# Kernel tuning notes

Hardware: AMD Instinct MI355X
Metric: run time of the kernel (lower is better)

Reference implementation:

```python
import jax, jax.numpy as jnp
import numpy as np

# ---- config (matches init_kwargs) ----
SPATIAL_SCALE = 0.0625
POOLED = 7
OUT_DIM = 256
SAMPLE_PER_PART = 4
TRANS_STD = 0.1
PART_SIZE = 7
DEFORM_FC_DIM = 1024
# group_size == 1 -> position-sensitive group index is always 0, channel c == ctop


def _deform_roi_pool(feat, rois, offset, no_trans):
    """Faithful JAX port of DeformablePSROIPoolForward (DCNv2), group_size=1.
    feat: (B,C,H,W), rois: (N,5)=[b,x1,y1,x2,y2], offset: (N,2,P,P) or None.
    Returns (N,C,P,P)."""
    B, C, H, W = feat.shape
    N = rois.shape[0]
    P, S = POOLED, SAMPLE_PER_PART
    dt = feat.dtype
    featT = jnp.transpose(feat, (0, 2, 3, 1))  # (B,H,W,C) for spatial gathers

    b = rois[:, 0].astype(jnp.int32)
    rsw = jnp.round(rois[:, 1]) * SPATIAL_SCALE - 0.5
    rsh = jnp.round(rois[:, 2]) * SPATIAL_SCALE - 0.5
    rew = (jnp.round(rois[:, 3]) + 1.0) * SPATIAL_SCALE - 0.5
    reh = (jnp.round(rois[:, 4]) + 1.0) * SPATIAL_SCALE - 0.5
    roi_w = jnp.maximum(rew - rsw, 0.1)
    roi_h = jnp.maximum(reh - rsh, 0.1)
    bin_h = roi_h / P            # (N,)
    bin_w = roi_w / P
    sub_h = bin_h / S
    sub_w = bin_w / S

    ph = jnp.arange(P)
    pw = jnp.arange(P)
    part_h = jnp.floor(ph.astype(dt) / P * PART_SIZE).astype(jnp.int32)  # == ph when part_size==P
    part_w = jnp.floor(pw.astype(dt) / P * PART_SIZE).astype(jnp.int32)

    if no_trans:
        tx = jnp.zeros((N, P, P), dt)
        ty = jnp.zeros((N, P, P), dt)
    else:
        tx = offset[:, 0][:, part_h][:, :, part_w] * TRANS_STD  # (N,P,P)
        ty = offset[:, 1][:, part_h][:, :, part_w] * TRANS_STD

    hstart = ph.astype(dt)[None, :, None] * bin_h[:, None, None] + rsh[:, None, None] + ty * roi_h[:, None, None]
    wstart = pw.astype(dt)[None, None, :] * bin_w[:, None, None] + rsw[:, None, None] + tx * roi_w[:, None, None]

    ih = jnp.arange(S).astype(dt)
    iw = jnp.arange(S).astype(dt)
    # sample coords, shape (N,P,P,S,S); ih along axis -2, iw along axis -1
    h = hstart[..., None, None] + ih[:, None] * sub_h[:, None, None, None, None]
    w = wstart[..., None, None] + iw[None, :] * sub_w[:, None, None, None, None]

    valid = (w >= -0.5) & (w <= W - 0.5) & (h >= -0.5) & (h <= H - 0.5)
    hc = jnp.clip(h, 0.0, H - 1.0)
    wc = jnp.clip(w, 0.0, W - 1.0)
    h0 = jnp.floor(hc).astype(jnp.int32)
    w0 = jnp.floor(wc).astype(jnp.int32)
    h1 = jnp.minimum(h0 + 1, H - 1)
    w1 = jnp.minimum(w0 + 1, W - 1)
    lh = hc - h0.astype(dt)
    lw = wc - w0.astype(dt)

    bidx = b[:, None, None, None, None]

    def g(yy, xx):  # (N,P,P,S,S,C)
        return featT[bidx, yy, xx]

    val = (g(h0, w0) * ((1 - lh) * (1 - lw))[..., None]
           + g(h0, w1) * ((1 - lh) * lw)[..., None]
           + g(h1, w0) * (lh * (1 - lw))[..., None]
           + g(h1, w1) * (lh * lw)[..., None])
    val = jnp.where(valid[..., None], val, jnp.zeros((), dt))
    ssum = val.sum(axis=(3, 4))                       # (N,P,P,C)
    cnt = valid.sum(axis=(3, 4)).astype(dt)           # (N,P,P)
    out = jnp.where(cnt[..., None] > 0, ssum / jnp.maximum(cnt, 1.0)[..., None], jnp.zeros((), dt))
    return jnp.transpose(out, (0, 3, 1, 2))           # (N,C,P,P)


def setup_inputs() -> dict:
    key = jax.random.key(0)
    ks = jax.random.split(key, 12)
    B, C, H, W = 2, OUT_DIM, 100, 100
    N = 512
    img = H / SPATIAL_SCALE  # 1600

    feat = jax.random.normal(ks[0], (B, C, H, W), jnp.float32)

    bi = jax.random.randint(ks[1], (N,), 0, B).astype(jnp.float32)
    x1 = jax.random.uniform(ks[2], (N,), jnp.float32, 0.0, img - 420.0)
    y1 = jax.random.uniform(ks[3], (N,), jnp.float32, 0.0, img - 420.0)
    x2 = x1 + jax.random.uniform(ks[4], (N,), jnp.float32, 32.0, 400.0)
    y2 = y1 + jax.random.uniform(ks[5], (N,), jnp.float32, 32.0, 400.0)
    rois = jnp.stack([bi, x1, y1, x2, y2], axis=1)

    fin = POOLED * POOLED * OUT_DIM  # 12544
    w1 = jax.random.normal(ks[6], (DEFORM_FC_DIM, fin), jnp.float32) / np.sqrt(fin)
    b1 = jnp.zeros((DEFORM_FC_DIM,), jnp.float32)
    w2 = jax.random.normal(ks[7], (DEFORM_FC_DIM, DEFORM_FC_DIM), jnp.float32) / np.sqrt(DEFORM_FC_DIM)
    b2 = jnp.zeros((DEFORM_FC_DIM,), jnp.float32)
    # original init zeroes the last layer; use small random so offsets/mask are non-trivial
    w3 = jax.random.normal(ks[8], (POOLED * POOLED * 3, DEFORM_FC_DIM), jnp.float32) * 0.01
    b3 = jnp.zeros((POOLED * POOLED * 3,), jnp.float32)
    return {"input": feat, "rois": rois, "w1": w1, "b1": b1, "w2": w2, "b2": b2, "w3": w3, "b3": b3}


def reference(input, rois, w1, b1, w2, b2, w3, b3):
    N = rois.shape[0]
    P = POOLED
    # pass 1: plain (no_trans) deformable RoI pooling to predict offsets/mask
    roi0 = _deform_roi_pool(input, rois, None, no_trans=True)      # (N,C,P,P)
    x = roi0.reshape(N, -1)
    x = jax.nn.relu(x @ w1.T + b1)
    x = jax.nn.relu(x @ w2.T + b2)
    om = (x @ w3.T + b3).reshape(N, 3, P, P)
    offset = om[:, 0:2]                                            # (N,2,P,P) [trans_x, trans_y]
    mask = jax.nn.sigmoid(om[:, 2:3])                              # (N,1,P,P)
    # pass 2: deformable pooling with learned offsets, modulated by mask
    out = _deform_roi_pool(input, rois, offset, no_trans=False) * mask
    return out
```

## Files before the change

kernel.cpp:

```cpp
#include <hip/hip_runtime.h>

#define BB 2
#define CC 256
#define HH 100
#define WW 100
#define NROI 512
#define KDIM 12544
#define FC 1024

typedef _Float16 half_t;
typedef _Float16 f16x2 __attribute__((ext_vector_type(2)));
typedef _Float16 f16x8 __attribute__((ext_vector_type(8)));
typedef _Float16 f16x4 __attribute__((ext_vector_type(4)));
typedef float f32x4 __attribute__((ext_vector_type(4)));

__device__ __forceinline__ void gload16(const half_t* g, half_t* l) {
  __builtin_amdgcn_global_load_lds(
      (const __attribute__((address_space(1))) unsigned int*)g,
      (__attribute__((address_space(3))) unsigned int*)l, 16, 0, 0);
}

__global__ __launch_bounds__(256) void prep0(const float* __restrict__ feat,
                                             half_t* __restrict__ featT,
                                             const float* __restrict__ w2,
                                             half_t* __restrict__ w2h) {
  int bid = blockIdx.x;
  if (bid >= 5008) {
    int i4 = ((bid - 5008) * 256 + threadIdx.x) * 4;
    float4 v = *(const float4*)(w2 + i4);
    f16x4 o;
    o[0] = (half_t)v.x; o[1] = (half_t)v.y; o[2] = (half_t)v.z; o[3] = (half_t)v.w;
    *(f16x4*)(w2h + i4) = o;
    return;
  }
  __shared__ float tile[32][33];
  const int bx = bid % 313;
  const int rem = bid / 313;
  const int by = rem & 7;
  const int bz = rem >> 3;
  const int tx = threadIdx.x & 31, ty = threadIdx.x >> 5;
  const int hw0 = bx * 32;
  const int c0 = by * 32;
  const float* fb = feat + (size_t)bz * CC * (HH * WW);
#pragma unroll
  for (int i = 0; i < 4; i++) {
    int c = c0 + ty + i * 8;
    int hw = hw0 + tx;
    tile[ty + i * 8][tx] = (hw < HH * WW) ? fb[(size_t)c * (HH * WW) + hw] : 0.0f;
  }
  __syncthreads();
  half_t* ob = featT + (size_t)bz * (HH * WW) * CC;
#pragma unroll
  for (int i = 0; i < 4; i++) {
    int hw = hw0 + ty + i * 8;
    int c = c0 + tx;
    if (hw < HH * WW) ob[(size_t)hw * CC + c] = (half_t)tile[tx][ty + i * 8];
  }
}

struct PixW { int idx; float w; };

template <bool PASS2>
__global__ __launch_bounds__(512) void pool_kernel(const half_t* __restrict__ featT,
                                                   const float* __restrict__ rois,
                                                   const float* __restrict__ part3,
                                                   const float* __restrict__ b3,
                                                   half_t* __restrict__ xout,
                                                   float* __restrict__ out,
                                                   const float* __restrict__ w1,
                                                   half_t* __restrict__ w1h) {
  __shared__ __align__(16) PixW s_pix[49 * 32];
  __shared__ int s_cnt[49];
  __shared__ float s_scale[49];
  __shared__ float  s_outf[PASS2 ? KDIM : 1];
  __shared__ half_t s_outh[PASS2 ? 1 : KDIM];

  const int n = blockIdx.x;
  const int tid = threadIdx.x;
  if (!PASS2 && n >= NROI) {
    int i4 = ((n - NROI) * 512 + tid) * 4;
    float4 v = *(const float4*)(w1 + i4);
    f16x4 o;
    o[0] = (half_t)v.x; o[1] = (half_t)v.y; o[2] = (half_t)v.z; o[3] = (half_t)v.w;
    *(f16x4*)(w1h + i4) = o;
    return;
  }
  const float* r = rois + n * 5;
  const int b = (int)r[0];
  const float rsw = rintf(r[1]) * 0.0625f - 0.5f;
  const float rsh = rintf(r[2]) * 0.0625f - 0.5f;
  const float rew = (rintf(r[3]) + 1.0f) * 0.0625f - 0.5f;
  const float reh = (rintf(r[4]) + 1.0f) * 0.0625f - 0.5f;
  const float roi_w = fmaxf(rew - rsw, 0.1f);
  const float roi_h = fmaxf(reh - rsh, 0.1f);
  const float bin_h = roi_h / 7.0f, bin_w = roi_w / 7.0f;
  const float sub_h = bin_h * 0.25f, sub_w = bin_w * 0.25f;
  const half_t* fb = featT + (size_t)b * (HH * WW) * CC;

  if (tid < 49) {
    const int p = tid, ph = p / 7, pw = p - ph * 7;
    float tx = 0.0f, ty = 0.0f, mask = 1.0f;
    if (PASS2) {
      float o0 = b3[p], o1 = b3[49 + p], o2 = b3[98 + p];
#pragma unroll
      for (int zz = 0; zz < 8; zz++) {
        const float* pz = part3 + ((size_t)zz * NROI + n) * 147;
        o0 += pz[p]; o1 += pz[49 + p]; o2 += pz[98 + p];
      }
      tx = o0 * 0.1f;
      ty = o1 * 0.1f;
      mask = 1.0f / (1.0f + expf(-o2));
    }
    const float hst = (float)ph * bin_h + rsh + ty * roi_h;
    const float wst = (float)pw * bin_w + rsw + tx * roi_w;
    float wh[6] = {0, 0, 0, 0, 0, 0};
    float hc0 = fminf(fmaxf(hst, 0.0f), 99.0f);
    const int r0 = (int)hc0;
    int rtop = r0;
    float vsh = 0.0f;
#pragma unroll
    for (int i = 0; i < 4; i++) {
      float h = hst + (float)i * sub_h;
      bool v = (h >= -0.5f) && (h <= (float)HH - 0.5f);
      float hc = fminf(fmaxf(h, 0.0f), 99.0f);
      int h0 = (int)hc;
      float lh = hc - (float)h0;
      int h1 = min(h0 + 1, HH - 1);
      if (v) { wh[h0 - r0] += 1.0f - lh; wh[h1 - r0] += lh; vsh += 1.0f; }
      rtop = h1;
    }
    float wwc[6] = {0, 0, 0, 0, 0, 0};
    float wc0 = fminf(fmaxf(wst, 0.0f), 99.0f);
    const int c0 = (int)wc0;
    int ctop = c0;
    float vsw = 0.0f;
#pragma unroll
    for (int j = 0; j < 4; j++) {
      float w = wst + (float)j * sub_w;
      bool v = (w >= -0.5f) && (w <= (float)WW - 0.5f);
      float wc = fminf(fmaxf(w, 0.0f), 99.0f);
      int w0 = (int)wc;
      float lw = wc - (float)w0;
      int w1_ = min(w0 + 1, WW - 1);
      if (v) { wwc[w0 - c0] += 1.0f - lw; wwc[w1_ - c0] += lw; vsw += 1.0f; }
      ctop = w1_;
    }
    const int nr = rtop - r0 + 1, nc = ctop - c0 + 1;
    float cntf = vsh * vsw;
    s_scale[p] = (cntf > 0.0f) ? mask / cntf : 0.0f;
    PixW* dst = &s_pix[p * 32];
    int m = 0;
    for (int ri = 0; ri < nr; ri++) {
      int rowoff = (r0 + ri) * WW + c0;
      for (int ci = 0; ci < nc; ci++) {
        dst[m].idx = (rowoff + ci) * CC;
        dst[m].w = wh[ri] * wwc[ci];
        m++;
      }
    }
    while (m & 15) { dst[m].idx = 0; dst[m].w = 0.0f; m++; }
    s_cnt[p] = m;
  }
  __syncthreads();

  const int wv = tid >> 6;
  const int lane = tid & 63;
  const int half = lane >> 5;
  const int c8 = (lane & 31) * 8;
  for (int p = wv; p < 49; p += 8) {
    const int cnt = s_cnt[p];
    const PixW* cp = &s_pix[p * 32];
    float a0 = 0, a1 = 0, a2 = 0, a3 = 0, a4 = 0, a5 = 0, a6 = 0, a7 = 0;
    for (int q = 0; q < cnt; q += 16) {
      PixW e0 = cp[q + 0 + half];
      PixW e1 = cp[q + 2 + half];
      PixW e2 = cp[q + 4 + half];
      PixW e3 = cp[q + 6 + half];
      PixW e4 = cp[q + 8 + half];
      PixW e5 = cp[q + 10 + half];
      PixW e6 = cp[q + 12 + half];
      PixW e7 = cp[q + 14 + half];
      f16x8 v0 = *(const f16x8*)(fb + e0.idx + c8);
      f16x8 v1 = *(const f16x8*)(fb + e1.idx + c8);
      f16x8 v2 = *(const f16x8*)(fb + e2.idx + c8);
      f16x8 v3 = *(const f16x8*)(fb + e3.idx + c8);
      f16x8 v4 = *(const f16x8*)(fb + e4.idx + c8);
      f16x8 v5 = *(const f16x8*)(fb + e5.idx + c8);
      f16x8 v6 = *(const f16x8*)(fb + e6.idx + c8);
      f16x8 v7 = *(const f16x8*)(fb + e7.idx + c8);
      a0 += e0.w * (float)v0[0] + e1.w * (float)v1[0] + e2.w * (float)v2[0] + e3.w * (float)v3[0]
          + e4.w * (float)v4[0] + e5.w * (float)v5[0] + e6.w * (float)v6[0] + e7.w * (float)v7[0];
      a1 += e0.w * (float)v0[1] + e1.w * (float)v1[1] + e2.w * (float)v2[1] + e3.w * (float)v3[1]
          + e4.w * (float)v4[1] + e5.w * (float)v5[1] + e6.w * (float)v6[1] + e7.w * (float)v7[1];
      a2 += e0.w * (float)v0[2] + e1.w * (float)v1[2] + e2.w * (float)v2[2] + e3.w * (float)v3[2]
          + e4.w * (float)v4[2] + e5.w * (float)v5[2] + e6.w * (float)v6[2] + e7.w * (float)v7[2];
      a3 += e0.w * (float)v0[3] + e1.w * (float)v1[3] + e2.w * (float)v2[3] + e3.w * (float)v3[3]
          + e4.w * (float)v4[3] + e5.w * (float)v5[3] + e6.w * (float)v6[3] + e7.w * (float)v7[3];
      a4 += e0.w * (float)v0[4] + e1.w * (float)v1[4] + e2.w * (float)v2[4] + e3.w * (float)v3[4]
          + e4.w * (float)v4[4] + e5.w * (float)v5[4] + e6.w * (float)v6[4] + e7.w * (float)v7[4];
      a5 += e0.w * (float)v0[5] + e1.w * (float)v1[5] + e2.w * (float)v2[5] + e3.w * (float)v3[5]
          + e4.w * (float)v4[5] + e5.w * (float)v5[5] + e6.w * (float)v6[5] + e7.w * (float)v7[5];
      a6 += e0.w * (float)v0[6] + e1.w * (float)v1[6] + e2.w * (float)v2[6] + e3.w * (float)v3[6]
          + e4.w * (float)v4[6] + e5.w * (float)v5[6] + e6.w * (float)v6[6] + e7.w * (float)v7[6];
      a7 += e0.w * (float)v0[7] + e1.w * (float)v1[7] + e2.w * (float)v2[7] + e3.w * (float)v3[7]
          + e4.w * (float)v4[7] + e5.w * (float)v5[7] + e6.w * (float)v6[7] + e7.w * (float)v7[7];
    }
    a0 += __shfl_xor(a0, 32); a1 += __shfl_xor(a1, 32);
    a2 += __shfl_xor(a2, 32); a3 += __shfl_xor(a3, 32);
    a4 += __shfl_xor(a4, 32); a5 += __shfl_xor(a5, 32);
    a6 += __shfl_xor(a6, 32); a7 += __shfl_xor(a7, 32);
    if (half == 0) {
      float sc = s_scale[p];
      a0 *= sc; a1 *= sc; a2 *= sc; a3 *= sc; a4 *= sc; a5 *= sc; a6 *= sc; a7 *= sc;
      if (PASS2) {
        s_outf[(c8 + 0) * 49 + p] = a0;
        s_outf[(c8 + 1) * 49 + p] = a1;
        s_outf[(c8 + 2) * 49 + p] = a2;
        s_outf[(c8 + 3) * 49 + p] = a3;
        s_outf[(c8 + 4) * 49 + p] = a4;
        s_outf[(c8 + 5) * 49 + p] = a5;
        s_outf[(c8 + 6) * 49 + p] = a6;
        s_outf[(c8 + 7) * 49 + p] = a7;
      } else {
        s_outh[(c8 + 0) * 49 + p] = (half_t)a0;
        s_outh[(c8 + 1) * 49 + p] = (half_t)a1;
        s_outh[(c8 + 2) * 49 + p] = (half_t)a2;
        s_outh[(c8 + 3) * 49 + p] = (half_t)a3;
        s_outh[(c8 + 4) * 49 + p] = (half_t)a4;
        s_outh[(c8 + 5) * 49 + p] = (half_t)a5;
        s_outh[(c8 + 6) * 49 + p] = (half_t)a6;
        s_outh[(c8 + 7) * 49 + p] = (half_t)a7;
      }
    }
  }
  __syncthreads();

  if (PASS2) {
    float* ob = out + (size_t)n * KDIM;
    for (int l = tid * 4; l < KDIM; l += 2048)
      *(float4*)(ob + l) = *(const float4*)(s_outf + l);
  } else {
    half_t* ob = xout + (size_t)n * KDIM;
    for (int l = tid * 8; l < KDIM; l += 4096)
      *(f16x8*)(ob + l) = *(const f16x8*)(s_outh + l);
  }
}

template <int SK>
__global__ __launch_bounds__(256, 2) void gemm_lds(const half_t* __restrict__ A,
                                                   const half_t* __restrict__ B,
                                                   float* __restrict__ P, int K) {
  __shared__ half_t As[2][128 * 64];
  __shared__ half_t Bs[2][128 * 64];
  const int d = blockIdx.x + gridDim.x * (blockIdx.y + gridDim.y * blockIdx.z);
  const int g = (d & 7) * (SK * 4) + (d >> 3);
  const int z = g >> 5;
  const int tile = g & 31;
  const int m0 = (tile & 3) * 128;
  const int n0 = (tile >> 2) * 128;
  const int Kc = K / SK;
  const int kbeg = z * Kc;
  const int tid = threadIdx.x;
  const int lane = tid & 63;
  const int wave = tid >> 6;
  const int wm = (wave & 1) * 64;
  const int wn = (wave >> 1) * 64;
  const int fr = lane & 15;
  const int kc0 = lane >> 4;
  const int lr = lane >> 3;
  const int lc = (lane & 7) ^ lr;
  const half_t* Ag = A + (size_t)(m0 + wave * 8 + lr) * K + kbeg + lc * 8;
  const half_t* Bg = B + (size_t)(n0 + wave * 8 + lr) * K + kbeg + lc * 8;
  f32x4 acc[4][4] = {};

  auto stage = [&](int buf, int ko) {
#pragma unroll
    for (int s = 0; s < 4; s++)
      gload16(Ag + (size_t)(32 * s) * K + ko, &As[buf][s * 2048 + wave * 512]);
#pragma unroll
    for (int s = 0; s < 4; s++)
      gload16(Bg + (size_t)(32 * s) * K + ko, &Bs[buf][s * 2048 + wave * 512]);
  };

  const int iters = Kc >> 6;
  stage(0, 0);
  if (iters > 1) {
    stage(1, 64);
    asm volatile("s_waitcnt vmcnt(8)" ::: "memory");
  } else {
    asm volatile("s_waitcnt vmcnt(0)" ::: "memory");
  }
  __builtin_amdgcn_s_barrier();

  for (int it = 0; it < iters; it++) {
    const int cur = it & 1;
#pragma unroll
    for (int ks = 0; ks < 2; ks++) {
      const int swz = ((kc0 + ks * 4) ^ (fr & 7)) * 8;
      f16x8 af[4], bf[4];
#pragma unroll
      for (int i = 0; i < 4; i++) af[i] = *(const f16x8*)&As[cur][(wm + i * 16 + fr) * 64 + swz];
#pragma unroll
      for (int j = 0; j < 4; j++) bf[j] = *(const f16x8*)&Bs[cur][(wn + j * 16 + fr) * 64 + swz];
      __builtin_amdgcn_s_setprio(1);
#pragma unroll
      for (int i = 0; i < 4; i++)
#pragma unroll
        for (int j = 0; j < 4; j++)
          acc[i][j] = __builtin_amdgcn_mfma_f32_16x16x32_f16(af[i], bf[j], acc[i][j], 0, 0, 0);
      __builtin_amdgcn_s_setprio(0);
    }
    asm volatile("s_waitcnt lgkmcnt(0)" ::: "memory");
    __builtin_amdgcn_s_barrier();
    const bool issue = (it + 2 < iters);
    if (issue) stage(cur, (it + 2) * 64);
    if (it + 1 < iters) {
      if (issue) asm volatile("s_waitcnt vmcnt(8)" ::: "memory");
      else       asm volatile("s_waitcnt vmcnt(0)" ::: "memory");
      __builtin_amdgcn_s_barrier();
    }
  }
  float* Pz = P + (((size_t)z * 32 + tile) * 4 + wave) * 4096;
#pragma unroll
  for (int i = 0; i < 4; i++)
#pragma unroll
    for (int j = 0; j < 4; j++)
#pragma unroll
      for (int rr = 0; rr < 4; rr++)
        Pz[((i * 4 + j) * 4 + rr) * 64 + lane] = acc[i][j][rr];
}

template <bool OUT16, bool RELU, int SK>
__global__ __launch_bounds__(256) void reduce_blocked(const float* __restrict__ P,
                                                      const float* __restrict__ bias,
                                                      void* __restrict__ out,
                                                      int MN, int N) {
  int i4 = (blockIdx.x * 256 + threadIdx.x) * 4;
  if (i4 >= MN) return;
  float4 s = *(const float4*)(P + i4);
#pragma unroll
  for (int z = 1; z < SK; z++) {
    float4 t = *(const float4*)(P + (size_t)z * MN + i4);
    s.x += t.x; s.y += t.y; s.z += t.z; s.w += t.w;
  }
  const int lane0 = i4 & 63;
  const int q     = (i4 >> 6) & 63;
  const int wave  = (i4 >> 12) & 3;
  const int bx    = (i4 >> 14) & 3;
  const int by    = (i4 >> 16) & 7;
  const int rr = q & 3, j_ = (q >> 2) & 3, i_ = q >> 4;
  const int row = bx * 128 + (wave & 1) * 64 + i_ * 16 + (lane0 >> 4) * 4 + rr;
  const int col = by * 128 + (wave >> 1) * 64 + j_ * 16 + (lane0 & 15);
  float4 bv = *(const float4*)(bias + col);
  s.x += bv.x; s.y += bv.y; s.z += bv.z; s.w += bv.w;
  if (RELU) {
    s.x = fmaxf(s.x, 0.0f); s.y = fmaxf(s.y, 0.0f);
    s.z = fmaxf(s.z, 0.0f); s.w = fmaxf(s.w, 0.0f);
  }
  size_t o = (size_t)row * N + col;
  if (OUT16) {
    f16x4 ov;
    ov[0] = (half_t)s.x; ov[1] = (half_t)s.y; ov[2] = (half_t)s.z; ov[3] = (half_t)s.w;
    *(f16x4*)((half_t*)out + o) = ov;
  } else {
    *(float4*)((float*)out + o) = s;
  }
}

__global__ __launch_bounds__(256) void gemm3_fused(const float* __restrict__ part2,
                                                   const float* __restrict__ b2,
                                                   const float* __restrict__ w3,
                                                   float* __restrict__ part3) {
  __shared__ float hs[8][128];
  const int n0 = blockIdx.x * 8;
  const int z3 = blockIdx.y;
  const int tid = threadIdx.x;
  const int MN = NROI * FC;
  {
    const int idx4 = tid * 4;
    const int nn = idx4 >> 7;
    const int kk = idx4 & 127;
    const int row = n0 + nn;
    const int col = z3 * 128 + kk;
    const int bx = (row >> 7) & 3;
    const int by = (col >> 7) & 7;
    const int wv = ((row >> 6) & 1) | (((col >> 6) & 1) << 1);
    const int q  = ((row >> 4) & 3) * 16 + ((col >> 4) & 3) * 4 + (row & 3);
    const int l0 = ((row >> 2) & 3) * 16 + (col & 15);
    const int tile = by * 4 + bx;
    const size_t base = (size_t)((tile * 4 + wv) * 4096 + q * 64 + l0);
    float4 s = *(const float4*)(part2 + base);
#pragma unroll
    for (int z2 = 1; z2 < 8; z2++) {
      float4 t = *(const float4*)(part2 + (size_t)z2 * MN + base);
      s.x += t.x; s.y += t.y; s.z += t.z; s.w += t.w;
    }
    float4 bv = *(const float4*)(b2 + col);
    s.x = fmaxf(s.x + bv.x, 0.0f);
    s.y = fmaxf(s.y + bv.y, 0.0f);
    s.z = fmaxf(s.z + bv.z, 0.0f);
    s.w = fmaxf(s.w + bv.w, 0.0f);
    *(float4*)(&hs[nn][kk]) = s;
  }
  __syncthreads();
  const int j = tid;
  if (j < 147) {
    const float* wr = w3 + (size_t)j * FC + z3 * 128;
    float acc[8] = {0, 0, 0, 0, 0, 0, 0, 0};
    for (int k = 0; k < 128; k += 4) {
      float4 wv = *(const float4*)(wr + k);
#pragma unroll
      for (int nn = 0; nn < 8; nn++)
        acc[nn] += hs[nn][k] * wv.x + hs[nn][k + 1] * wv.y +
                   hs[nn][k + 2] * wv.z + hs[nn][k + 3] * wv.w;
    }
#pragma unroll
    for (int nn = 0; nn < 8; nn++)
      part3[((size_t)z3 * NROI + n0 + nn) * 147 + j] = acc[nn];
  }
}

extern "C" void kernel_launch(void* const* d_in, const int* in_sizes, int n_in,
                              void* d_out, int out_size, void* d_ws, size_t ws_size,
                              hipStream_t stream) {
  const float* feat = (const float*)d_in[0];
  const float* rois = (const float*)d_in[1];
  const float* w1 = (const float*)d_in[2];
  const float* b1 = (const float*)d_in[3];
  const float* w2 = (const float*)d_in[4];
  const float* b2 = (const float*)d_in[5];
  const float* w3 = (const float*)d_in[6];
  const float* b3 = (const float*)d_in[7];
  float* out = (float*)d_out;
  char* ws = (char*)d_ws;

  half_t* featT = (half_t*)ws;
  half_t* xh    = (half_t*)(ws + 10240000);
  half_t* w1h   = (half_t*)(ws + 23085056);
  half_t* w2h   = (half_t*)(ws + 48775168);
  half_t* h1    = (half_t*)(ws + 50872320);
  float*  part  = (float*)(ws + 54319104);
  float*  part3 = (float*)(ws + 83679232);

  const int MN = NROI * FC;

  prep0<<<dim3(6032), dim3(256), 0, stream>>>(feat, featT, w2, w2h);

  pool_kernel<false><<<dim3(NROI + 6272), dim3(512), 0, stream>>>(
      featT, rois, nullptr, nullptr, xh, nullptr, w1, w1h);

  gemm_lds<14><<<dim3(4, 8, 14), dim3(256), 0, stream>>>(xh, w1h, part, KDIM);
  reduce_blocked<true, true, 14><<<dim3(MN / 1024), dim3(256), 0, stream>>>(part, b1, (void*)h1, MN, FC);

  gemm_lds<8><<<dim3(4, 8, 8), dim3(256), 0, stream>>>(h1, w2h, part, FC);

  gemm3_fused<<<dim3(64, 8), dim3(256), 0, stream>>>(part, b2, w3, part3);
  pool_kernel<true><<<dim3(NROI), dim3(512), 0, stream>>>(
      featT, rois, part3, b3, nullptr, out, nullptr, nullptr);
}
```

Before: 215.8 us.

## Sort RoIs by batch and spatial center to improve cache locality in pooling

```diff
diff --git a/kernel.cpp b/kernel.cpp
--- a/kernel.cpp
+++ b/kernel.cpp
@@ -23,8 +23,40 @@
 __global__ __launch_bounds__(256) void prep0(const float* __restrict__ feat,
                                              half_t* __restrict__ featT,
                                              const float* __restrict__ w2,
-                                             half_t* __restrict__ w2h) {
+                                             half_t* __restrict__ w2h,
+                                             const float* __restrict__ rois,
+                                             int* __restrict__ perm) {
   int bid = blockIdx.x;
+  if (bid == 6032) {
+    __shared__ unsigned s_sv[512];
+    for (int i = threadIdx.x; i < 512; i += 256) {
+      const float* rr = rois + i * 5;
+      int bb = (int)rr[0];
+      float cxf = (rr[1] + rr[3]) * 0.03125f;
+      float cyf = (rr[2] + rr[4]) * 0.03125f;
+      int cx = min(127, max(0, (int)cxf));
+      int cy = min(127, max(0, (int)cyf));
+      unsigned key = ((unsigned)bb << 14) | ((unsigned)cy << 7) | (unsigned)cx;
+      s_sv[i] = (key << 9) | (unsigned)i;
+    }
+    __syncthreads();
+    for (int ksz = 2; ksz <= 512; ksz <<= 1) {
+      for (int jsz = ksz >> 1; jsz > 0; jsz >>= 1) {
+        for (int i = threadIdx.x; i < 512; i += 256) {
+          int ixj = i ^ jsz;
+          if (ixj > i) {
+            unsigned a = s_sv[i], c = s_sv[ixj];
+            bool up = ((i & ksz) == 0);
+            if ((a > c) == up) { s_sv[i] = c; s_sv[ixj] = a; }
+          }
+        }
+        __syncthreads();
+      }
+    }
+    for (int i = threadIdx.x; i < 512; i += 256)
+      perm[i] = (int)(s_sv[i] & 511u);
+    return;
+  }
   if (bid >= 5008) {
     int i4 = ((bid - 5008) * 256 + threadIdx.x) * 4;
     float4 v = *(const float4*)(w2 + i4);
@@ -68,23 +100,25 @@
                                                    half_t* __restrict__ xout,
                                                    float* __restrict__ out,
                                                    const float* __restrict__ w1,
-                                                   half_t* __restrict__ w1h) {
+                                                   half_t* __restrict__ w1h,
+                                                   const int* __restrict__ perm) {
   __shared__ __align__(16) PixW s_pix[49 * 32];
   __shared__ int s_cnt[49];
   __shared__ float s_scale[49];
   __shared__ float  s_outf[PASS2 ? KDIM : 1];
   __shared__ half_t s_outh[PASS2 ? 1 : KDIM];
 
-  const int n = blockIdx.x;
+  const int bidx = blockIdx.x;
   const int tid = threadIdx.x;
-  if (!PASS2 && n >= NROI) {
-    int i4 = ((n - NROI) * 512 + tid) * 4;
+  if (!PASS2 && bidx >= NROI) {
+    int i4 = ((bidx - NROI) * 512 + tid) * 4;
     float4 v = *(const float4*)(w1 + i4);
     f16x4 o;
     o[0] = (half_t)v.x; o[1] = (half_t)v.y; o[2] = (half_t)v.z; o[3] = (half_t)v.w;
     *(f16x4*)(w1h + i4) = o;
     return;
   }
+  const int n = perm[((bidx & 7) << 6) | (bidx >> 3)];
   const float* r = rois + n * 5;
   const int b = (int)r[0];
   const float rsw = rintf(r[1]) * 0.0625f - 0.5f;
@@ -441,13 +475,14 @@
   half_t* h1    = (half_t*)(ws + 50872320);
   float*  part  = (float*)(ws + 54319104);
   float*  part3 = (float*)(ws + 83679232);
+  int*    perm  = (int*)(ws + 86087680);
 
   const int MN = NROI * FC;
 
-  prep0<<<dim3(6032), dim3(256), 0, stream>>>(feat, featT, w2, w2h);
+  prep0<<<dim3(6033), dim3(256), 0, stream>>>(feat, featT, w2, w2h, rois, perm);
 
   pool_kernel<false><<<dim3(NROI + 6272), dim3(512), 0, stream>>>(
-      featT, rois, nullptr, nullptr, xh, nullptr, w1, w1h);
+      featT, rois, nullptr, nullptr, xh, nullptr, w1, w1h, perm);
 
   gemm_lds<14><<<dim3(4, 8, 14), dim3(256), 0, stream>>>(xh, w1h, part, KDIM);
   reduce_blocked<true, true, 14><<<dim3(MN / 1024), dim3(256), 0, stream>>>(part, b1, (void*)h1, MN, FC);
@@ -456,5 +491,5 @@
 
   gemm3_fused<<<dim3(64, 8), dim3(256), 0, stream>>>(part, b2, w3, part3);
   pool_kernel<true><<<dim3(NROI), dim3(512), 0, stream>>>(
-      featT, rois, part3, b3, nullptr, out, nullptr, nullptr);
-}
+      featT, rois, part3, b3, nullptr, out, nullptr, nullptr, perm);
+}
```

Result: slower. 228.9 us (+6.1%).
